# Kernel optimization log

Hardware: AMD Instinct MI355X
Metric: run time of the kernel (lower is better)

Reference implementation:

```python
import jax, jax.numpy as jnp
import numpy as np

B, T, H = 64, 2048, 64  # basins, daily timesteps, MLP hidden width


def _mlp(x, W1, b1, W2, b2, W3, b3, W4, b4):
    # x: [..., 4] -> [..., 5]; tanh hidden layers, linear head
    h = jnp.tanh(x @ W1 + b1)
    h = jnp.tanh(h @ W2 + b2)
    h = jnp.tanh(h @ W3 + b3)
    return h @ W4 + b4


def _step(x):
    # smooth step function from the torch module
    return (jnp.tanh(5.0 * x) + 1.0) * 0.5


def _interp(series, t):
    # linear interpolation of per-basin forcing series [B, T] at scalar time t
    # (time grid is the integer daily grid 0..T-1, matching time_series)
    n = series.shape[1]
    i0 = jnp.clip(jnp.floor(t).astype(jnp.int32), 0, n - 2)
    frac = t - i0.astype(series.dtype)
    pair = jax.lax.dynamic_slice_in_dim(series, i0, 2, axis=1)  # [B, 2]
    return pair[:, 0] * (1.0 - frac) + pair[:, 1] * frac


def _forward(s_snow, s_water, precp_series, tmean_series, lday_series, time_series,
             W1, b1, W2, b2, W3, b3, W4, b4):
    params = (W1, b1, W2, b2, W3, b3, W4, b4)

    def rhs(t, y):  # y: [B, 2]
        s0, s1 = y[:, 0], y[:, 1]
        precp = _interp(precp_series, t)
        temp = _interp(tmean_series, t)
        lday = _interp(lday_series, t)
        o = _mlp(jnp.stack([s0, s1, precp, temp], axis=-1), *params)  # [B, 5]
        # scale_target_vars=True branch
        p_snow = jax.nn.relu(jnp.sinh(o[:, 0]) * _step(-temp))
        p_rain = jax.nn.relu(jnp.sinh(o[:, 1]))
        m = jax.nn.relu(_step(s0) * jnp.sinh(o[:, 2]))
        et = _step(s1) * jnp.exp(o[:, 3]) * lday
        q = _step(s1) * jnp.exp(o[:, 4])
        return jnp.stack([p_snow - m, p_rain + m - et - q], axis=-1)

    y0 = jnp.stack([s_snow[:, 0], s_water[:, 0]], axis=-1)  # [B, 2]
    t0s = time_series[:-1]
    dts = time_series[1:] - time_series[:-1]

    def scan_step(y, td):  # classic RK4 between consecutive grid points
        t0, dt = td
        half = dt * 0.5
        k1 = rhs(t0, y)
        k2 = rhs(t0 + half, y + half * k1)
        k3 = rhs(t0 + half, y + half * k2)
        k4 = rhs(t0 + dt, y + dt * k3)
        y_next = y + (dt / 6.0) * (k1 + 2.0 * k2 + 2.0 * k3 + k4)
        return y_next, y_next

    _, ys = jax.lax.scan(scan_step, y0, (t0s, dts))  # [T-1, B, 2]
    y_full = jnp.concatenate([y0[None], ys], axis=0)  # [T, B, 2]
    y_full = jnp.transpose(y_full, (1, 0, 2))  # [B, T, 2]

    # final NN pass over the integrated states + raw forcing series
    inputs_nn = jnp.stack(
        [y_full[..., 0], y_full[..., 1], precp_series, tmean_series], axis=-1)  # [B, T, 4]
    q_out = _mlp(inputs_nn, *params)[..., -1]  # [B, T] (last output column = q)
    return q_out


def setup_inputs() -> dict:
    key = jax.random.key(0)
    ks = jax.random.split(key, 9)
    return {
        "s_snow": jax.random.uniform(ks[0], (B, T), dtype=jnp.float32),
        "s_water": jax.random.uniform(ks[1], (B, T), dtype=jnp.float32),
        "precp_series": jax.random.uniform(ks[2], (B, T), dtype=jnp.float32),
        "tmean_series": jax.random.normal(ks[3], (B, T), dtype=jnp.float32),
        "lday_series": jax.random.uniform(ks[4], (B, T), dtype=jnp.float32) * 0.5,
        "time_series": jnp.arange(T, dtype=jnp.float32),
        "W1": jax.random.normal(ks[5], (4, H), dtype=jnp.float32) / jnp.sqrt(4.0),
        "b1": jnp.zeros((H,), jnp.float32),
        "W2": jax.random.normal(ks[6], (H, H), dtype=jnp.float32) / jnp.sqrt(float(H)),
        "b2": jnp.zeros((H,), jnp.float32),
        "W3": jax.random.normal(ks[7], (H, H), dtype=jnp.float32) / jnp.sqrt(float(H)),
        "b3": jnp.zeros((H,), jnp.float32),
        "W4": jax.random.normal(ks[8], (H, 5), dtype=jnp.float32) * (0.1 / jnp.sqrt(float(H))),
        "b4": jnp.zeros((5,), jnp.float32),
    }


def reference(s_snow, s_water, precp_series, tmean_series, lday_series, time_series,
              W1, b1, W2, b2, W3, b3, W4, b4):
    return _forward(s_snow, s_water, precp_series, tmean_series, lday_series,
                    time_series, W1, b1, W2, b2, W3, b3, W4, b4)
```

## Files before the change

kernel.cpp:

```cpp
#include <hip/hip_runtime.h>
#include <cmath>

#define LOG2E 1.44269504088896340736f
#define TMAX 2048

#if __has_builtin(__builtin_amdgcn_exp2f)
#define EXP2F(x) __builtin_amdgcn_exp2f(x)
#else
#define EXP2F(x) exp2f(x)
#endif
#if __has_builtin(__builtin_amdgcn_rcpf)
#define RCPF(x) __builtin_amdgcn_rcpf(x)
#else
#define RCPF(x) (1.0f / (x))
#endif

typedef float float2v __attribute__((ext_vector_type(2)));
typedef float float4v __attribute__((ext_vector_type(4)));

__device__ __forceinline__ float fexp(float x)  { return EXP2F(x * LOG2E); }
__device__ __forceinline__ float ftanh(float x) { return 1.0f - 2.0f * RCPF(1.0f + EXP2F(x * (2.0f * LOG2E))); }
__device__ __forceinline__ float fstep(float x) { return RCPF(1.0f + EXP2F(x * (-10.0f * LOG2E))); }
__device__ __forceinline__ float fsinh(float x) { float e = fexp(x); return 0.5f * (e - RCPF(e)); }

__device__ __forceinline__ int fadd_i(int a, int b) {
    return __builtin_bit_cast(int, __builtin_bit_cast(float, a) + __builtin_bit_cast(float, b));
}

__device__ __forceinline__ float wave_sum63(float x) {
    int v = __builtin_bit_cast(int, x);
    v = fadd_i(v, __builtin_amdgcn_update_dpp(0, v, 0x111, 0xF, 0xF, true));
    v = fadd_i(v, __builtin_amdgcn_update_dpp(0, v, 0x112, 0xF, 0xF, true));
    v = fadd_i(v, __builtin_amdgcn_update_dpp(0, v, 0x114, 0xF, 0xF, true));
    v = fadd_i(v, __builtin_amdgcn_update_dpp(0, v, 0x118, 0xF, 0xF, true));
    v = fadd_i(v, __builtin_amdgcn_update_dpp(0, v, 0x142, 0xA, 0xF, true));
    v = fadd_i(v, __builtin_amdgcn_update_dpp(0, v, 0x143, 0xC, 0xF, true));
    return __builtin_bit_cast(float, v);
}

__device__ __forceinline__ float quad_sum(float x) {
    int v = __builtin_bit_cast(int, x);
    v = fadd_i(v, __builtin_amdgcn_update_dpp(0, v, 0xB1, 0xF, 0xF, true));
    v = fadd_i(v, __builtin_amdgcn_update_dpp(0, v, 0x4E, 0xF, 0xF, true));
    return __builtin_bit_cast(float, v);
}

__device__ __forceinline__ float rl(float x, int l) {
    return __builtin_bit_cast(float, __builtin_amdgcn_readlane(__builtin_bit_cast(int, x), l));
}

__device__ __forceinline__ float2v pk_fma(float2v a, float2v b, float2v c) {
    float2v d;
    asm("v_pk_fma_f32 %0, %1, %2, %3" : "=v"(d) : "v"(a), "v"(b), "v"(c));
    return d;
}

__device__ __forceinline__ float2v vlo(float4v v) { return __builtin_shufflevector(v, v, 0, 1); }
__device__ __forceinline__ float2v vhi(float4v v) { return __builtin_shufflevector(v, v, 2, 3); }

__device__ __forceinline__ void barrier_lgkm() {
    asm volatile("s_waitcnt lgkmcnt(0)" ::: "memory");
    __builtin_amdgcn_s_barrier();
    asm volatile("" ::: "memory");
}

__global__ __launch_bounds__(256, 1)
void exphydro_kernel(const float* __restrict__ g_snow, const float* __restrict__ g_water,
                     const float* __restrict__ g_pr, const float* __restrict__ g_tm,
                     const float* __restrict__ g_ld, const float* __restrict__ g_t,
                     const float* __restrict__ W1, const float* __restrict__ b1,
                     const float* __restrict__ W2, const float* __restrict__ b2,
                     const float* __restrict__ W3, const float* __restrict__ b3,
                     const float* __restrict__ W4, const float* __restrict__ b4,
                     float* __restrict__ out, int T)
{
    const int tid  = threadIdx.x;
    const int lane = tid & 63;
    const int wid  = tid >> 6;
    const int b    = blockIdx.x;
    const int qk   = lane & 3;
    const int qo   = lane >> 2;
    const int col2 = 16 * wid + qo;

    __shared__ __align__(16) float4v s_f[TMAX];
    __shared__ __align__(16) float hc[4][64];
    __shared__ __align__(16) float partAB[2][4][64];

    for (int i = tid; i < T; i += 256) {
        s_f[i] = float4v{g_pr[b * T + i], g_tm[b * T + i], g_ld[b * T + i], g_t[i]};
    }

    float w1r[4];
#pragma unroll
    for (int j = 0; j < 4; ++j) w1r[j] = W1[j * 64 + lane];
    float b1v = b1[lane];
    float2v w2n[8];
#pragma unroll
    for (int k = 0; k < 8; ++k) {
        int r = qk * 16 + 2 * k;
        w2n[k] = float2v{W2[r * 64 + col2], W2[(r + 1) * 64 + col2]};
    }
    float b2s = b2[col2];
    float w3f[16];
#pragma unroll
    for (int k = 0; k < 16; ++k) w3f[k] = W3[(16 * wid + k) * 64 + lane];
    float b3v = (wid == 0) ? b3[lane] : 0.0f;
    float w4r[5], b4r[5];
#pragma unroll
    for (int k = 0; k < 5; ++k) { w4r[k] = W4[lane * 5 + k]; b4r[k] = b4[k]; }

    __syncthreads();

    auto mlp_o63 = [&](float h1, float (*part)[64], float* o) {
        hc[wid][lane] = h1;
        const float* hq = &hc[wid][qk * 16];
        float4v q0 = *reinterpret_cast<const float4v*>(hq + 0);
        float4v q1 = *reinterpret_cast<const float4v*>(hq + 4);
        float4v q2 = *reinterpret_cast<const float4v*>(hq + 8);
        float4v q3 = *reinterpret_cast<const float4v*>(hq + 12);
        float2v a0 = float2v{0.0f, 0.0f}, a1 = float2v{0.0f, 0.0f};
        a0 = pk_fma(w2n[0], vlo(q0), a0); a1 = pk_fma(w2n[1], vhi(q0), a1);
        a0 = pk_fma(w2n[2], vlo(q1), a0); a1 = pk_fma(w2n[3], vhi(q1), a1);
        a0 = pk_fma(w2n[4], vlo(q2), a0); a1 = pk_fma(w2n[5], vhi(q2), a1);
        a0 = pk_fma(w2n[6], vlo(q3), a0); a1 = pk_fma(w2n[7], vhi(q3), a1);
        float2v sa = a0 + a1;
        float t2 = quad_sum(sa.x + sa.y);
        float h2 = ftanh(t2 + b2s);
        float c0 = b3v, c1 = 0.0f, c2 = 0.0f, c3 = 0.0f;
#pragma unroll
        for (int j = 0; j < 16; j += 4) {
            float s0 = rl(h2, 4 * j);
            float s1 = rl(h2, 4 * (j + 1));
            float s2 = rl(h2, 4 * (j + 2));
            float s3 = rl(h2, 4 * (j + 3));
            c0 = fmaf(w3f[j + 0], s0, c0);
            c1 = fmaf(w3f[j + 1], s1, c1);
            c2 = fmaf(w3f[j + 2], s2, c2);
            c3 = fmaf(w3f[j + 3], s3, c3);
        }
        part[wid][lane] = (c0 + c1) + (c2 + c3);
        barrier_lgkm();
        float h3 = ftanh((part[0][lane] + part[1][lane]) + (part[2][lane] + part[3][lane]));
#pragma unroll
        for (int k = 0; k < 5; ++k) o[k] = wave_sum63(w4r[k] * h3) + b4r[k];
    };

    auto rhs = [&](float base, float y0v, float y1v, float ld, float snt,
                   float (*part)[64], float& d0, float& d1, float& o4) {
        float step0 = fstep(y0v);
        float st1   = fstep(y1v);
        float h1 = ftanh(fmaf(w1r[0], y0v, fmaf(w1r[1], y1v, base)));
        float o[5];
        mlp_o63(h1, part, o);
        float psnow = fmaxf(0.0f, fsinh(o[0]) * snt);
        float prain = fmaxf(0.0f, fsinh(o[1]));
        float melt  = fmaxf(0.0f, step0 * fsinh(o[2]));
        float eq    = st1 * fmaf(fexp(o[3]), ld, fexp(o[4]));
        float d0l = psnow - melt;
        float d1l = (prain + melt) - eq;
        d0 = rl(d0l, 63);
        d1 = rl(d1l, 63);
        o4 = o[4];
    };

    float y0v = g_snow[b * T];
    float y1v = g_water[b * T];

    for (int st = 0; st < T - 1; ++st) {
        float4v fc = s_f[st];
        float4v fn = s_f[st + 1];

        float dt = fn.w - fc.w, half = 0.5f * dt, c6 = dt * (1.0f / 6.0f);
        float prH = 0.5f * (fc.x + fn.x);
        float tmH = 0.5f * (fc.y + fn.y);
        float ldH = 0.5f * (fc.z + fn.z);
        float snA = fstep(-fc.y), snH = fstep(-tmH), snC = fstep(-fn.y);
        float baseA = fmaf(w1r[2], fc.x, fmaf(w1r[3], fc.y, b1v));
        float baseH = fmaf(w1r[2], prH,  fmaf(w1r[3], tmH,  b1v));
        float baseC = fmaf(w1r[2], fn.x, fmaf(w1r[3], fn.y, b1v));

        float k1a, k1b, k2a, k2b, k3a, k3b, k4a, k4b, o4a, o4x;
        rhs(baseA, y0v, y1v, fc.z, snA, partAB[0], k1a, k1b, o4a);
        if (tid == 63) out[b * T + st] = o4a;
        rhs(baseH, fmaf(half, k1a, y0v), fmaf(half, k1b, y1v), ldH, snH, partAB[1], k2a, k2b, o4x);
        rhs(baseH, fmaf(half, k2a, y0v), fmaf(half, k2b, y1v), ldH, snH, partAB[0], k3a, k3b, o4x);
        rhs(baseC, fmaf(dt, k3a, y0v),   fmaf(dt, k3b, y1v),   fn.z, snC, partAB[1], k4a, k4b, o4x);

        y0v = fmaf(c6, (k1a + k4a) + 2.0f * (k2a + k3a), y0v);
        y1v = fmaf(c6, (k1b + k4b) + 2.0f * (k2b + k3b), y1v);
    }

    {
        float4v fL = s_f[T - 1];
        float base = fmaf(w1r[2], fL.x, fmaf(w1r[3], fL.y, b1v));
        float h1 = ftanh(fmaf(w1r[0], y0v, fmaf(w1r[1], y1v, base)));
        float o[5];
        mlp_o63(h1, partAB[0], o);
        if (tid == 63) out[b * T + (T - 1)] = o[4];
    }
}

extern "C" void kernel_launch(void* const* d_in, const int* in_sizes, int n_in,
                              void* d_out, int out_size, void* d_ws, size_t ws_size,
                              hipStream_t stream) {
    const float* g_snow  = (const float*)d_in[0];
    const float* g_water = (const float*)d_in[1];
    const float* g_pr    = (const float*)d_in[2];
    const float* g_tm    = (const float*)d_in[3];
    const float* g_ld    = (const float*)d_in[4];
    const float* g_t     = (const float*)d_in[5];
    const float* W1 = (const float*)d_in[6];
    const float* b1 = (const float*)d_in[7];
    const float* W2 = (const float*)d_in[8];
    const float* b2 = (const float*)d_in[9];
    const float* W3 = (const float*)d_in[10];
    const float* b3 = (const float*)d_in[11];
    const float* W4 = (const float*)d_in[12];
    const float* b4 = (const float*)d_in[13];

    const int T = in_sizes[5];
    const int B = in_sizes[0] / T;

    exphydro_kernel<<<dim3(B), dim3(256), 0, stream>>>(
        g_snow, g_water, g_pr, g_tm, g_ld, g_t,
        W1, b1, W2, b2, W3, b3, W4, b4,
        (float*)d_out, T);
}
```

Baseline: 4.808 ms.

## Replace LDS-staged layer-2 matvec with DPP broadcast and cross-row permlane reductions

```diff
diff --git a/kernel.cpp b/kernel.cpp
--- a/kernel.cpp
+++ b/kernel.cpp
@@ -15,7 +15,6 @@
 #define RCPF(x) (1.0f / (x))
 #endif
 
-typedef float float2v __attribute__((ext_vector_type(2)));
 typedef float float4v __attribute__((ext_vector_type(4)));
 
 __device__ __forceinline__ float fexp(float x)  { return EXP2F(x * LOG2E); }
@@ -38,25 +37,33 @@
     return __builtin_bit_cast(float, v);
 }
 
-__device__ __forceinline__ float quad_sum(float x) {
-    int v = __builtin_bit_cast(int, x);
-    v = fadd_i(v, __builtin_amdgcn_update_dpp(0, v, 0xB1, 0xF, 0xF, true));
-    v = fadd_i(v, __builtin_amdgcn_update_dpp(0, v, 0x4E, 0xF, 0xF, true));
-    return __builtin_bit_cast(float, v);
-}
-
 __device__ __forceinline__ float rl(float x, int l) {
     return __builtin_bit_cast(float, __builtin_amdgcn_readlane(__builtin_bit_cast(int, x), l));
 }
 
-__device__ __forceinline__ float2v pk_fma(float2v a, float2v b, float2v c) {
-    float2v d;
-    asm("v_pk_fma_f32 %0, %1, %2, %3" : "=v"(d) : "v"(a), "v"(b), "v"(c));
-    return d;
-}
-
-__device__ __forceinline__ float2v vlo(float4v v) { return __builtin_shufflevector(v, v, 0, 1); }
-__device__ __forceinline__ float2v vhi(float4v v) { return __builtin_shufflevector(v, v, 2, 3); }
+__device__ __forceinline__ float rowpair16_sum(float x) {
+    float a = x, b = x;
+    asm("v_permlane16_swap_b32 %0, %1" : "+v"(a), "+v"(b));
+    return a + b;
+}
+__device__ __forceinline__ float rowpair32_sum(float x) {
+    float a = x, b = x;
+    asm("v_permlane32_swap_b32 %0, %1" : "+v"(a), "+v"(b));
+    return a + b;
+}
+__device__ __forceinline__ float cls4_sum(float x) {
+    float s = rowpair32_sum(rowpair16_sum(x));
+    int v = __builtin_bit_cast(int, s);
+    v = fadd_i(v, __builtin_amdgcn_update_dpp(0, v, 0x114, 0xF, 0xF, true));
+    v = fadd_i(v, __builtin_amdgcn_update_dpp(0, v, 0x118, 0xF, 0xF, true));
+    return __builtin_bit_cast(float, v);
+}
+
+template <int I>
+__device__ __forceinline__ float quad_bcast(float x) {
+    return __builtin_bit_cast(float,
+        __builtin_amdgcn_update_dpp(0, __builtin_bit_cast(int, x), I * 0x55, 0xF, 0xF, true));
+}
 
 __device__ __forceinline__ void barrier_lgkm() {
     asm volatile("s_waitcnt lgkmcnt(0)" ::: "memory");
@@ -78,12 +85,10 @@
     const int lane = tid & 63;
     const int wid  = tid >> 6;
     const int b    = blockIdx.x;
-    const int qk   = lane & 3;
-    const int qo   = lane >> 2;
-    const int col2 = 16 * wid + qo;
+    const int q4   = lane >> 2;
+    const int j4   = lane & 3;
 
     __shared__ __align__(16) float4v s_f[TMAX];
-    __shared__ __align__(16) float hc[4][64];
     __shared__ __align__(16) float partAB[2][4][64];
 
     for (int i = tid; i < T; i += 256) {
@@ -94,13 +99,14 @@
 #pragma unroll
     for (int j = 0; j < 4; ++j) w1r[j] = W1[j * 64 + lane];
     float b1v = b1[lane];
-    float2v w2n[8];
-#pragma unroll
-    for (int k = 0; k < 8; ++k) {
-        int r = qk * 16 + 2 * k;
-        w2n[k] = float2v{W2[r * 64 + col2], W2[(r + 1) * 64 + col2]};
-    }
-    float b2s = b2[col2];
+    float w2q[4][4], b2q[4];
+#pragma unroll
+    for (int m = 0; m < 4; ++m) {
+#pragma unroll
+        for (int i = 0; i < 4; ++i)
+            w2q[m][i] = W2[(4 * q4 + i) * 64 + 16 * wid + 4 * m + j4];
+        b2q[m] = b2[16 * wid + 4 * m + j4];
+    }
     float w3f[16];
 #pragma unroll
     for (int k = 0; k < 16; ++k) w3f[k] = W3[(16 * wid + k) * 64 + lane];
@@ -112,32 +118,34 @@
     __syncthreads();
 
     auto mlp_o63 = [&](float h1, float (*part)[64], float* o) {
-        hc[wid][lane] = h1;
-        const float* hq = &hc[wid][qk * 16];
-        float4v q0 = *reinterpret_cast<const float4v*>(hq + 0);
-        float4v q1 = *reinterpret_cast<const float4v*>(hq + 4);
-        float4v q2 = *reinterpret_cast<const float4v*>(hq + 8);
-        float4v q3 = *reinterpret_cast<const float4v*>(hq + 12);
-        float2v a0 = float2v{0.0f, 0.0f}, a1 = float2v{0.0f, 0.0f};
-        a0 = pk_fma(w2n[0], vlo(q0), a0); a1 = pk_fma(w2n[1], vhi(q0), a1);
-        a0 = pk_fma(w2n[2], vlo(q1), a0); a1 = pk_fma(w2n[3], vhi(q1), a1);
-        a0 = pk_fma(w2n[4], vlo(q2), a0); a1 = pk_fma(w2n[5], vhi(q2), a1);
-        a0 = pk_fma(w2n[6], vlo(q3), a0); a1 = pk_fma(w2n[7], vhi(q3), a1);
-        float2v sa = a0 + a1;
-        float t2 = quad_sum(sa.x + sa.y);
-        float h2 = ftanh(t2 + b2s);
+        float h10 = quad_bcast<0>(h1), h11 = quad_bcast<1>(h1),
+              h12 = quad_bcast<2>(h1), h13 = quad_bcast<3>(h1);
+        float t0 = fmaf(w2q[0][3], h13, fmaf(w2q[0][2], h12, fmaf(w2q[0][1], h11, w2q[0][0] * h10)));
+        float t1 = fmaf(w2q[1][3], h13, fmaf(w2q[1][2], h12, fmaf(w2q[1][1], h11, w2q[1][0] * h10)));
+        float t2 = fmaf(w2q[2][3], h13, fmaf(w2q[2][2], h12, fmaf(w2q[2][1], h11, w2q[2][0] * h10)));
+        float t3 = fmaf(w2q[3][3], h13, fmaf(w2q[3][2], h12, fmaf(w2q[3][1], h11, w2q[3][0] * h10)));
+        t0 = cls4_sum(t0); t1 = cls4_sum(t1); t2 = cls4_sum(t2); t3 = cls4_sum(t3);
+        float g0 = ftanh(t0 + b2q[0]);
+        float g1 = ftanh(t1 + b2q[1]);
+        float g2 = ftanh(t2 + b2q[2]);
+        float g3 = ftanh(t3 + b2q[3]);
         float c0 = b3v, c1 = 0.0f, c2 = 0.0f, c3 = 0.0f;
-#pragma unroll
-        for (int j = 0; j < 16; j += 4) {
-            float s0 = rl(h2, 4 * j);
-            float s1 = rl(h2, 4 * (j + 1));
-            float s2 = rl(h2, 4 * (j + 2));
-            float s3 = rl(h2, 4 * (j + 3));
-            c0 = fmaf(w3f[j + 0], s0, c0);
-            c1 = fmaf(w3f[j + 1], s1, c1);
-            c2 = fmaf(w3f[j + 2], s2, c2);
-            c3 = fmaf(w3f[j + 3], s3, c3);
-        }
+        c0 = fmaf(w3f[ 0], rl(g0, 12), c0);
+        c1 = fmaf(w3f[ 1], rl(g0, 13), c1);
+        c2 = fmaf(w3f[ 2], rl(g0, 14), c2);
+        c3 = fmaf(w3f[ 3], rl(g0, 15), c3);
+        c0 = fmaf(w3f[ 4], rl(g1, 12), c0);
+        c1 = fmaf(w3f[ 5], rl(g1, 13), c1);
+        c2 = fmaf(w3f[ 6], rl(g1, 14), c2);
+        c3 = fmaf(w3f[ 7], rl(g1, 15), c3);
+        c0 = fmaf(w3f[ 8], rl(g2, 12), c0);
+        c1 = fmaf(w3f[ 9], rl(g2, 13), c1);
+        c2 = fmaf(w3f[10], rl(g2, 14), c2);
+        c3 = fmaf(w3f[11], rl(g2, 15), c3);
+        c0 = fmaf(w3f[12], rl(g3, 12), c0);
+        c1 = fmaf(w3f[13], rl(g3, 13), c1);
+        c2 = fmaf(w3f[14], rl(g3, 14), c2);
+        c3 = fmaf(w3f[15], rl(g3, 15), c3);
         part[wid][lane] = (c0 + c1) + (c2 + c3);
         barrier_lgkm();
         float h3 = ftanh((part[0][lane] + part[1][lane]) + (part[2][lane] + part[3][lane]));
```

Result: slower. 5.394 ms (+12.2%).

## Pack two basins per 512-thread block to interleave serial RK4 chains

Applied to the files above, without the earlier changes.

```diff
diff --git a/kernel.cpp b/kernel.cpp
--- a/kernel.cpp
+++ b/kernel.cpp
@@ -64,7 +64,7 @@
     asm volatile("" ::: "memory");
 }
 
-__global__ __launch_bounds__(256, 1)
+__global__ __launch_bounds__(512, 1)
 void exphydro_kernel(const float* __restrict__ g_snow, const float* __restrict__ g_water,
                      const float* __restrict__ g_pr, const float* __restrict__ g_tm,
                      const float* __restrict__ g_ld, const float* __restrict__ g_t,
@@ -72,23 +72,39 @@
                      const float* __restrict__ W2, const float* __restrict__ b2,
                      const float* __restrict__ W3, const float* __restrict__ b3,
                      const float* __restrict__ W4, const float* __restrict__ b4,
-                     float* __restrict__ out, int T)
+                     float* __restrict__ out, int T, int B)
 {
     const int tid  = threadIdx.x;
     const int lane = tid & 63;
     const int wid  = tid >> 6;
-    const int b    = blockIdx.x;
+    const int samp = wid >> 2;
+    const int wq   = wid & 3;
+    const int b0   = 2 * blockIdx.x;
+    const int bs   = (b0 + samp < B) ? (b0 + samp) : (B - 1);
     const int qk   = lane & 3;
     const int qo   = lane >> 2;
-    const int col2 = 16 * wid + qo;
-
-    __shared__ __align__(16) float4v s_f[TMAX];
-    __shared__ __align__(16) float hc[4][64];
-    __shared__ __align__(16) float partAB[2][4][64];
-
-    for (int i = tid; i < T; i += 256) {
-        s_f[i] = float4v{g_pr[b * T + i], g_tm[b * T + i], g_ld[b * T + i], g_t[i]};
-    }
+    const int col2 = 16 * wq + qo;
+
+    __shared__ float s_pr[2][TMAX];
+    __shared__ float s_tm[2][TMAX];
+    __shared__ float s_ld[2][TMAX];
+    __shared__ __align__(16) float hc[8][64];
+    __shared__ __align__(16) float partAB[2][2][4][64];
+
+    {
+        const int sh = tid >> 8;
+        const int to = tid & 255;
+        const int bb = (b0 + sh < B) ? (b0 + sh) : (B - 1);
+        for (int j = to; j < T; j += 256) {
+            s_pr[sh][j] = g_pr[bb * T + j];
+            s_tm[sh][j] = g_tm[bb * T + j];
+            s_ld[sh][j] = g_ld[bb * T + j];
+        }
+    }
+
+    const float dtg  = g_t[1] - g_t[0];
+    const float half = 0.5f * dtg;
+    const float c6   = dtg * (1.0f / 6.0f);
 
     float w1r[4];
 #pragma unroll
@@ -103,8 +119,8 @@
     float b2s = b2[col2];
     float w3f[16];
 #pragma unroll
-    for (int k = 0; k < 16; ++k) w3f[k] = W3[(16 * wid + k) * 64 + lane];
-    float b3v = (wid == 0) ? b3[lane] : 0.0f;
+    for (int k = 0; k < 16; ++k) w3f[k] = W3[(16 * wq + k) * 64 + lane];
+    float b3v = (wq == 0) ? b3[lane] : 0.0f;
     float w4r[5], b4r[5];
 #pragma unroll
     for (int k = 0; k < 5; ++k) { w4r[k] = W4[lane * 5 + k]; b4r[k] = b4[k]; }
@@ -138,7 +154,7 @@
             c2 = fmaf(w3f[j + 2], s2, c2);
             c3 = fmaf(w3f[j + 3], s3, c3);
         }
-        part[wid][lane] = (c0 + c1) + (c2 + c3);
+        part[wq][lane] = (c0 + c1) + (c2 + c3);
         barrier_lgkm();
         float h3 = ftanh((part[0][lane] + part[1][lane]) + (part[2][lane] + part[3][lane]));
 #pragma unroll
@@ -163,40 +179,45 @@
         o4 = o[4];
     };
 
-    float y0v = g_snow[b * T];
-    float y1v = g_water[b * T];
+    float y0v = g_snow[bs * T];
+    float y1v = g_water[bs * T];
+
+    const float* pr = s_pr[samp];
+    const float* tm = s_tm[samp];
+    const float* ld = s_ld[samp];
+    float (*pA)[64] = partAB[samp][0];
+    float (*pB)[64] = partAB[samp][1];
 
     for (int st = 0; st < T - 1; ++st) {
-        float4v fc = s_f[st];
-        float4v fn = s_f[st + 1];
-
-        float dt = fn.w - fc.w, half = 0.5f * dt, c6 = dt * (1.0f / 6.0f);
-        float prH = 0.5f * (fc.x + fn.x);
-        float tmH = 0.5f * (fc.y + fn.y);
-        float ldH = 0.5f * (fc.z + fn.z);
-        float snA = fstep(-fc.y), snH = fstep(-tmH), snC = fstep(-fn.y);
-        float baseA = fmaf(w1r[2], fc.x, fmaf(w1r[3], fc.y, b1v));
-        float baseH = fmaf(w1r[2], prH,  fmaf(w1r[3], tmH,  b1v));
-        float baseC = fmaf(w1r[2], fn.x, fmaf(w1r[3], fn.y, b1v));
+        float prc = pr[st], prn = pr[st + 1];
+        float tmc = tm[st], tmn = tm[st + 1];
+        float ldc = ld[st], ldn = ld[st + 1];
+
+        float prH = 0.5f * (prc + prn);
+        float tmH = 0.5f * (tmc + tmn);
+        float ldH = 0.5f * (ldc + ldn);
+        float snA = fstep(-tmc), snH = fstep(-tmH), snC = fstep(-tmn);
+        float baseA = fmaf(w1r[2], prc, fmaf(w1r[3], tmc, b1v));
+        float baseH = fmaf(w1r[2], prH, fmaf(w1r[3], tmH, b1v));
+        float baseC = fmaf(w1r[2], prn, fmaf(w1r[3], tmn, b1v));
 
         float k1a, k1b, k2a, k2b, k3a, k3b, k4a, k4b, o4a, o4x;
-        rhs(baseA, y0v, y1v, fc.z, snA, partAB[0], k1a, k1b, o4a);
-        if (tid == 63) out[b * T + st] = o4a;
-        rhs(baseH, fmaf(half, k1a, y0v), fmaf(half, k1b, y1v), ldH, snH, partAB[1], k2a, k2b, o4x);
-        rhs(baseH, fmaf(half, k2a, y0v), fmaf(half, k2b, y1v), ldH, snH, partAB[0], k3a, k3b, o4x);
-        rhs(baseC, fmaf(dt, k3a, y0v),   fmaf(dt, k3b, y1v),   fn.z, snC, partAB[1], k4a, k4b, o4x);
+        rhs(baseA, y0v, y1v, ldc, snA, pA, k1a, k1b, o4a);
+        if (wq == 0 && lane == 63) out[bs * T + st] = o4a;
+        rhs(baseH, fmaf(half, k1a, y0v), fmaf(half, k1b, y1v), ldH, snH, pB, k2a, k2b, o4x);
+        rhs(baseH, fmaf(half, k2a, y0v), fmaf(half, k2b, y1v), ldH, snH, pA, k3a, k3b, o4x);
+        rhs(baseC, fmaf(dtg,  k3a, y0v), fmaf(dtg,  k3b, y1v), ldn, snC, pB, k4a, k4b, o4x);
 
         y0v = fmaf(c6, (k1a + k4a) + 2.0f * (k2a + k3a), y0v);
         y1v = fmaf(c6, (k1b + k4b) + 2.0f * (k2b + k3b), y1v);
     }
 
     {
-        float4v fL = s_f[T - 1];
-        float base = fmaf(w1r[2], fL.x, fmaf(w1r[3], fL.y, b1v));
+        float base = fmaf(w1r[2], pr[T - 1], fmaf(w1r[3], tm[T - 1], b1v));
         float h1 = ftanh(fmaf(w1r[0], y0v, fmaf(w1r[1], y1v, base)));
         float o[5];
-        mlp_o63(h1, partAB[0], o);
-        if (tid == 63) out[b * T + (T - 1)] = o[4];
+        mlp_o63(h1, pA, o);
+        if (wq == 0 && lane == 63) out[bs * T + (T - 1)] = o[4];
     }
 }
 
@@ -220,9 +241,10 @@
 
     const int T = in_sizes[5];
     const int B = in_sizes[0] / T;
-
-    exphydro_kernel<<<dim3(B), dim3(256), 0, stream>>>(
+    const int nblk = (B + 1) / 2;
+
+    exphydro_kernel<<<dim3(nblk), dim3(512), 0, stream>>>(
         g_snow, g_water, g_pr, g_tm, g_ld, g_t,
         W1, b1, W2, b2, W3, b3, W4, b4,
-        (float*)d_out, T);
-}
+        (float*)d_out, T, B);
+}
```

New measurement: 6.931 ms. 44.2% more time.
